# Kernel optimization log

Measured on AMD Instinct MI355X. Metric: run time of the kernel, lower is better.

Reference implementation:

```python
import jax, jax.numpy as jnp
import numpy as np

N_DIMS = 4
NEG_SLOPE = 0.01
ALPHA = 0.5

def leaky(v):
    return jnp.where(v > 0, v, NEG_SLOPE * v)

def gcn_conv(h, W, b, edge_index, n):
    """PyG GCNConv: add self-loops, symmetric normalization, then aggregate."""
    hw = h @ W  # [N, H]
    loops = jnp.arange(n, dtype=edge_index.dtype)
    src = jnp.concatenate([edge_index[0], loops])
    dst = jnp.concatenate([edge_index[1], loops])
    deg = jax.ops.segment_sum(jnp.ones_like(dst, dtype=hw.dtype), dst, num_segments=n)
    dinv = jnp.where(deg > 0, jax.lax.rsqrt(deg), 0.0)
    norm = dinv[src] * dinv[dst]  # [E+N]
    out = jax.ops.segment_sum(hw[src] * norm[:, None], dst, num_segments=n)
    return out + b

def setup_inputs() -> dict:
    key = jax.random.key(0)
    ks = jax.random.split(key, 8)
    N, IN, H, OUT, E = 50000, 512, 256, 512, 800000
    def kaiming(k, shape, fan_in):
        bound = np.sqrt(6.0 / fan_in)  # kaiming_uniform a=sqrt(5)-ish approx; gain sqrt(2)/sqrt(fan_in)*sqrt(3)
        bound = np.sqrt(2.0) * np.sqrt(3.0 / fan_in)
        return jax.random.uniform(k, shape, jnp.float32, -bound, bound)
    x = jax.random.normal(ks[0], (N, IN), jnp.float32)
    all_dim_edge_index = jax.random.randint(ks[1], (N_DIMS, 2, E), 0, N, jnp.int64)
    proj_mat = kaiming(ks[2], (N_DIMS, IN, H), IN)
    gcn_W = jax.random.uniform(ks[3], (N_DIMS, H, H), jnp.float32, -1, 1) * np.sqrt(1.0 / H)
    gcn_b = jnp.zeros((N_DIMS, H), jnp.float32)
    bilinear = kaiming(ks[4], (H, H), H)
    fan = H * N_DIMS
    inv_W = jax.random.uniform(ks[5], (fan, OUT), jnp.float32, -np.sqrt(1.0 / fan), np.sqrt(1.0 / fan))
    inv_b = jax.random.uniform(ks[6], (OUT,), jnp.float32, -np.sqrt(1.0 / fan), np.sqrt(1.0 / fan))
    return {"x": x, "all_dim_edge_index": all_dim_edge_index, "proj_mat": proj_mat,
            "gcn_W": gcn_W, "gcn_b": gcn_b, "bilinear": bilinear, "inv_W": inv_W, "inv_b": inv_b}

def reference(x, all_dim_edge_index, proj_mat, gcn_W, gcn_b, bilinear, inv_W, inv_b):
    n = x.shape[0]
    # per-dimension projection: [n_dims, N, H]
    dim_repr = leaky(jnp.einsum('ni,dih->dnh', x, proj_mat))
    # within-dimension GCN message passing (loop over small fixed n_dims)
    within_aggr = jnp.stack([
        gcn_conv(dim_repr[d], gcn_W[d], gcn_b[d], all_dim_edge_index[d], n)
        for d in range(N_DIMS)])
    # cross-dimension attention
    attention = jnp.einsum('aji,ik,bjk->ab', proj_mat, bilinear, proj_mat)
    attention = jax.nn.softmax(attention, axis=0)
    across_aggr = jnp.einsum('ab,anh->bnh', attention, dim_repr)
    new_dim_repr = ALPHA * within_aggr + (1.0 - ALPHA) * across_aggr  # [n_dims, N, H]
    concat = jnp.transpose(new_dim_repr, (1, 0, 2)).reshape(n, -1)  # [N, n_dims*H]
    return leaky(concat @ inv_W + inv_b)
```

## Files before the change

### kernel.cpp

```cpp
#include <hip/hip_runtime.h>
#include <math.h>

constexpr int N_NODES = 50000;
constexpr int IN_F    = 512;
constexpr int H_F     = 256;
constexpr int OUT_F   = 512;
constexpr int N_EDGE  = 800000;
constexpr int NDIM    = 4;
constexpr long NH     = (long)N_NODES * H_F;

#define LEAKY_SLOPE 0.01f

__device__ __forceinline__ float leaky_f(float v) { return v > 0.0f ? v : LEAKY_SLOPE * v; }

typedef __bf16 bf16x8 __attribute__((ext_vector_type(8)));
typedef float  f32x4  __attribute__((ext_vector_type(4)));

__device__ __forceinline__ void gload16(const void* g, void* s) {
  __builtin_amdgcn_global_load_lds(
      (const __attribute__((address_space(1))) void*)g,
      (__attribute__((address_space(3))) void*)s, 16, 0, 0);
}

template<bool AF32>
__global__ __launch_bounds__(256) void gemm_k(
    const float* __restrict__ Af, int ldaf,
    const __bf16* __restrict__ A1h, const __bf16* __restrict__ A1l, int lda1,
    const __bf16* __restrict__ A2h, const __bf16* __restrict__ A2l, int lda2, int kSplit,
    const __bf16* __restrict__ BhT, const __bf16* __restrict__ BlT,
    float* __restrict__ C, int ldc,
    const float* __restrict__ biasVec,
    __bf16* __restrict__ Oh, __bf16* __restrict__ Ol, int ldo,
    int M, int N, int K, int accumulate, int leaky)
{
  __shared__ __bf16 Ash[128][32];
  __shared__ __bf16 Asl[128][32];
  __shared__ __bf16 Bsh[128][32];
  __shared__ __bf16 Bsl[128][32];

  const int tid  = threadIdx.x;
  const int lane = tid & 63;
  const int wid  = tid >> 6;
  const int wm   = wid & 1;
  const int wn   = wid >> 1;
  const int l15  = lane & 15;
  const int quad = lane >> 4;
  const int col0 = blockIdx.x * 128;
  const int row0 = blockIdx.y * 128;

  f32x4 acc[4][4] = {};
  const int nkt = K >> 5;

  for (int kt = 0; kt < nkt; ++kt) {
    const int kk = kt << 5;
    __syncthreads();

    if constexpr (AF32) {
      #pragma unroll
      for (int p = 0; p < 4; ++p) {
        const int m = (tid >> 3) + p * 32;
        int row = row0 + m; row = row < M ? row : M - 1;
        const float4 v = *(const float4*)(Af + (size_t)row * ldaf + kk + (tid & 7) * 4);
        const float f[4] = {v.x, v.y, v.z, v.w};
        union { __bf16 b[4]; short4 s; } hh, ll;
        #pragma unroll
        for (int i = 0; i < 4; ++i) {
          const __bf16 hb = (__bf16)f[i];
          hh.b[i] = hb;
          ll.b[i] = (__bf16)(f[i] - (float)hb);
        }
        *(short4*)&Ash[m][(tid & 7) * 4] = hh.s;
        *(short4*)&Asl[m][(tid & 7) * 4] = ll.s;
      }
    } else {
      const __bf16* Ah; const __bf16* Al; int lda, k0;
      if (kk < kSplit) { Ah = A1h; Al = A1l; lda = lda1; k0 = kk; }
      else             { Ah = A2h; Al = A2l; lda = lda2; k0 = kk - kSplit; }
      #pragma unroll
      for (int p = 0; p < 2; ++p) {
        const int c = tid + p * 256;
        int row = row0 + (c >> 2); row = row < M ? row : M - 1;
        const size_t go = (size_t)row * lda + k0 + (c & 3) * 8;
        gload16(Ah + go, (__bf16*)Ash + (size_t)c * 8);
        gload16(Al + go, (__bf16*)Asl + (size_t)c * 8);
      }
    }
    #pragma unroll
    for (int p = 0; p < 2; ++p) {
      const int c = tid + p * 256;
      const int nn = col0 + (c >> 2);
      const size_t go = (size_t)nn * K + kk + (c & 3) * 8;
      gload16(BhT + go, (__bf16*)Bsh + (size_t)c * 8);
      gload16(BlT + go, (__bf16*)Bsl + (size_t)c * 8);
    }
    __syncthreads();

    bf16x8 ah[4], al[4], bh[4], bl[4];
    #pragma unroll
    for (int t = 0; t < 4; ++t) {
      ah[t] = *(const bf16x8*)&Ash[wm * 64 + t * 16 + l15][quad * 8];
      al[t] = *(const bf16x8*)&Asl[wm * 64 + t * 16 + l15][quad * 8];
      bh[t] = *(const bf16x8*)&Bsh[wn * 64 + t * 16 + l15][quad * 8];
      bl[t] = *(const bf16x8*)&Bsl[wn * 64 + t * 16 + l15][quad * 8];
    }
    #pragma unroll
    for (int mt = 0; mt < 4; ++mt)
      #pragma unroll
      for (int nt = 0; nt < 4; ++nt) {
        acc[mt][nt] = __builtin_amdgcn_mfma_f32_16x16x32_bf16(ah[mt], bh[nt], acc[mt][nt], 0, 0, 0);
        acc[mt][nt] = __builtin_amdgcn_mfma_f32_16x16x32_bf16(ah[mt], bl[nt], acc[mt][nt], 0, 0, 0);
        acc[mt][nt] = __builtin_amdgcn_mfma_f32_16x16x32_bf16(al[mt], bh[nt], acc[mt][nt], 0, 0, 0);
      }
  }

  #pragma unroll
  for (int mt = 0; mt < 4; ++mt)
    #pragma unroll
    for (int nt = 0; nt < 4; ++nt) {
      const int col = col0 + wn * 64 + nt * 16 + l15;
      const float bv = biasVec ? biasVec[col] : 0.0f;
      #pragma unroll
      for (int r = 0; r < 4; ++r) {
        const int row = row0 + wm * 64 + mt * 16 + quad * 4 + r;
        if (row < M) {
          float v = acc[mt][nt][r] + bv;
          if (accumulate) v += C[(size_t)row * ldc + col];
          if (leaky) v = leaky_f(v);
          if (Oh) {
            const __bf16 hv = (__bf16)v;
            Oh[(size_t)row * ldo + col] = hv;
            Ol[(size_t)row * ldo + col] = (__bf16)(v - (float)hv);
          } else {
            C[(size_t)row * ldc + col] = v;
          }
        }
      }
    }
}

__global__ void splitT_kernel(const float* __restrict__ B, __bf16* __restrict__ h,
                              __bf16* __restrict__ l, int Kd, int Nd, int total)
{
  int i = blockIdx.x * 256 + threadIdx.x;
  if (i >= total) return;
  int z   = i / (Kd * Nd);
  int rem = i - z * (Kd * Nd);
  int k = rem / Nd;
  int n = rem - k * Nd;
  float v = B[i];
  __bf16 hv = (__bf16)v;
  long o = (long)z * Kd * Nd + (long)n * Kd + k;
  h[o] = hv;
  l[o] = (__bf16)(v - (float)hv);
}

__global__ void splitA_kernel(const float* __restrict__ A, __bf16* __restrict__ h,
                              __bf16* __restrict__ l, long total)
{
  long i = (long)blockIdx.x * 256 + threadIdx.x;
  if (i >= total) return;
  float v = A[i];
  __bf16 hv = (__bf16)v;
  h[i] = hv;
  l[i] = (__bf16)(v - (float)hv);
}

__global__ void bcat_kernel(const float* __restrict__ invW, const float* __restrict__ att,
                            __bf16* __restrict__ h, __bf16* __restrict__ l)
{
  int i = blockIdx.x * 256 + threadIdx.x;
  if (i >= NDIM * OUT_F * 512) return;
  int d   = i >> 18;
  int rem = i & 262143;
  int n = rem >> 9;
  int k = rem & 511;
  float v;
  if (k < H_F) {
    v = invW[(long)(d * H_F + k) * OUT_F + n];
  } else {
    float s = 0.f;
    #pragma unroll
    for (int b = 0; b < 4; ++b)
      s += att[d * 4 + b] * invW[(long)(b * H_F + (k - H_F)) * OUT_F + n];
    v = 0.5f * s;
  }
  __bf16 hv = (__bf16)v;
  h[i] = hv;
  l[i] = (__bf16)(v - (float)hv);
}

__global__ void deg_count_kernel(const int* __restrict__ edges, int* __restrict__ cnt, int E)
{
  int i = blockIdx.x * 256 + threadIdx.x;
  if (i >= NDIM * E) return;
  int d = i / E;
  int e = i - d * E;
  int t = edges[(long)d * 2 * E + E + e];
  atomicAdd(&cnt[d * N_NODES + t], 1);
}

__global__ __launch_bounds__(1024) void scan_kernel(const int* __restrict__ cnt,
                                                    int* __restrict__ row_start,
                                                    float* __restrict__ dinv)
{
  const int d    = blockIdx.x;
  const int tid  = threadIdx.x;
  const int lane = tid & 63;
  const int wid  = tid >> 6;
  __shared__ int wsum[16];
  __shared__ int carry_s;
  if (tid == 0) carry_s = 0;
  __syncthreads();
  for (int base = 0; base < N_NODES; base += 1024) {
    int i = base + tid;
    int v = (i < N_NODES) ? cnt[d * N_NODES + i] : 0;
    if (i < N_NODES) dinv[d * N_NODES + i] = sqrtf(0.5f / (float)(v + 1));
    int incl = v;
    #pragma unroll
    for (int off = 1; off < 64; off <<= 1) {
      int nb = __shfl_up(incl, off, 64);
      if (lane >= off) incl += nb;
    }
    if (lane == 63) wsum[wid] = incl;
    __syncthreads();
    if (wid == 0 && lane < 16) {
      int s = wsum[lane];
      #pragma unroll
      for (int off = 1; off < 16; off <<= 1) {
        int nb = __shfl_up(s, off, 16);
        if (lane >= off) s += nb;
      }
      wsum[lane] = s;
    }
    __syncthreads();
    int waveoff = (wid == 0) ? 0 : wsum[wid - 1];
    if (i < N_NODES) row_start[d * (N_NODES + 1) + i] = carry_s + waveoff + incl - v;
    __syncthreads();
    if (tid == 1023) carry_s += wsum[15];
    __syncthreads();
  }
  if (tid == 0) row_start[d * (N_NODES + 1) + N_NODES] = carry_s;
}

__global__ void fill_kernel(const int* __restrict__ edges, const int* __restrict__ row_start,
                            int* __restrict__ fill_cnt, int* __restrict__ csr_src, int E)
{
  int i = blockIdx.x * 256 + threadIdx.x;
  if (i >= NDIM * E) return;
  int d = i / E;
  int e = i - d * E;
  int s = edges[(long)d * 2 * E + e];
  int t = edges[(long)d * 2 * E + E + e];
  int pos = row_start[d * (N_NODES + 1) + t] + atomicAdd(&fill_cnt[d * N_NODES + t], 1);
  csr_src[(long)d * E + pos] = s;
}

__global__ __launch_bounds__(256) void gather_aggr_kernel(
    const float* __restrict__ hw, const int* __restrict__ csr_src,
    const int* __restrict__ row_start, const float* __restrict__ dinv,
    const float* __restrict__ bias, __bf16* __restrict__ Wh, __bf16* __restrict__ Wl)
{
  const int n = blockIdx.x * 4 + (threadIdx.x >> 6);
  const int lane = threadIdx.x & 63;
  const float dt = dinv[n];
  const float sl = dt * dt;
  const float4 b = *(const float4*)(bias + lane * 4);
  const float4 h = *(const float4*)(hw + (size_t)n * H_F + lane * 4);
  float4 a0 = make_float4(0.5f * b.x + sl * h.x, 0.5f * b.y + sl * h.y,
                          0.5f * b.z + sl * h.z, 0.5f * b.w + sl * h.w);
  float4 a1 = make_float4(0.f, 0.f, 0.f, 0.f);
  const int beg = row_start[n];
  const int end = row_start[n + 1];
  int j = beg;
  for (; j + 2 <= end; j += 2) {
    const int s0 = csr_src[j];
    const int s1 = csr_src[j + 1];
    const float nm0 = dt * dinv[s0];
    const float nm1 = dt * dinv[s1];
    const float4 v0 = *(const float4*)(hw + (size_t)s0 * H_F + lane * 4);
    const float4 v1 = *(const float4*)(hw + (size_t)s1 * H_F + lane * 4);
    a0.x = fmaf(nm0, v0.x, a0.x); a0.y = fmaf(nm0, v0.y, a0.y);
    a0.z = fmaf(nm0, v0.z, a0.z); a0.w = fmaf(nm0, v0.w, a0.w);
    a1.x = fmaf(nm1, v1.x, a1.x); a1.y = fmaf(nm1, v1.y, a1.y);
    a1.z = fmaf(nm1, v1.z, a1.z); a1.w = fmaf(nm1, v1.w, a1.w);
  }
  if (j < end) {
    const int s0 = csr_src[j];
    const float nm0 = dt * dinv[s0];
    const float4 v0 = *(const float4*)(hw + (size_t)s0 * H_F + lane * 4);
    a0.x = fmaf(nm0, v0.x, a0.x); a0.y = fmaf(nm0, v0.y, a0.y);
    a0.z = fmaf(nm0, v0.z, a0.z); a0.w = fmaf(nm0, v0.w, a0.w);
  }
  const float av[4] = {a0.x + a1.x, a0.y + a1.y, a0.z + a1.z, a0.w + a1.w};
  union { __bf16 b[4]; short4 s; } H, L;
  #pragma unroll
  for (int i = 0; i < 4; ++i) {
    const __bf16 hv = (__bf16)av[i];
    H.b[i] = hv;
    L.b[i] = (__bf16)(av[i] - (float)hv);
  }
  *(short4*)(Wh + (size_t)n * H_F + lane * 4) = H.s;
  *(short4*)(Wl + (size_t)n * H_F + lane * 4) = L.s;
}

__global__ void att_dot_kernel(const float* __restrict__ T, const float* __restrict__ P,
                               float* __restrict__ out16)
{
  const int a = blockIdx.x >> 2;
  const int b = blockIdx.x & 3;
  const float* ta = T + (long)a * (IN_F * H_F);
  const float* pb = P + (long)b * (IN_F * H_F);
  float s = 0.f;
  for (int i = threadIdx.x; i < IN_F * H_F; i += 256) s += ta[i] * pb[i];
  #pragma unroll
  for (int off = 32; off > 0; off >>= 1) s += __shfl_down(s, off, 64);
  __shared__ float red[4];
  if ((threadIdx.x & 63) == 0) red[threadIdx.x >> 6] = s;
  __syncthreads();
  if (threadIdx.x == 0) out16[blockIdx.x] = red[0] + red[1] + red[2] + red[3];
}

__global__ void att_softmax_kernel(const float* __restrict__ raw, float* __restrict__ att)
{
  int b = threadIdx.x;
  if (b < 4) {
    float r0 = raw[b], r1 = raw[4 + b], r2 = raw[8 + b], r3 = raw[12 + b];
    float m = fmaxf(fmaxf(r0, r1), fmaxf(r2, r3));
    float e0 = expf(r0 - m), e1 = expf(r1 - m), e2 = expf(r2 - m), e3 = expf(r3 - m);
    float inv = 1.0f / (e0 + e1 + e2 + e3);
    att[b] = e0 * inv; att[4 + b] = e1 * inv; att[8 + b] = e2 * inv; att[12 + b] = e3 * inv;
  }
}

extern "C" void kernel_launch(void* const* d_in, const int* in_sizes, int n_in,
                              void* d_out, int out_size, void* d_ws, size_t ws_size,
                              hipStream_t stream)
{
  const float* x     = (const float*)d_in[0];
  const int*   edges = (const int*)d_in[1];
  const float* proj  = (const float*)d_in[2];
  const float* gcnW  = (const float*)d_in[3];
  const float* gcnB  = (const float*)d_in[4];
  const float* bil   = (const float*)d_in[5];
  const float* invW  = (const float*)d_in[6];
  const float* invB  = (const float*)d_in[7];
  float* out = (float*)d_out;

  float* HWB       = (float*)d_ws;
  float* dinv      = HWB + NH;
  float* Tbuf      = dinv + NDIM * N_NODES;
  float* att_raw   = Tbuf + (long)NDIM * IN_F * H_F;
  float* att       = att_raw + 16;
  int*   cnt       = (int*)(att + 16);
  int*   fill_cnt  = cnt + NDIM * N_NODES;
  int*   row_start = fill_cnt + NDIM * N_NODES;
  int*   csr_src   = row_start + NDIM * (N_NODES + 1);
  __bf16* projTh   = (__bf16*)(csr_src + (long)NDIM * N_EDGE);
  __bf16* projTl   = projTh + (long)NDIM * IN_F * H_F;
  __bf16* gcnWTh   = projTl + (long)NDIM * IN_F * H_F;
  __bf16* gcnWTl   = gcnWTh + (long)NDIM * H_F * H_F;
  __bf16* bcatTh   = gcnWTl + (long)NDIM * H_F * H_F;
  __bf16* bcatTl   = bcatTh + (long)NDIM * OUT_F * 512;
  __bf16* bilTh    = bcatTl + (long)NDIM * OUT_F * 512;
  __bf16* bilTl    = bilTh + (long)H_F * H_F;
  __bf16* Rh       = bilTl + (long)H_F * H_F;
  __bf16* Rl       = Rh + NH;
  __bf16* WBh      = Rl + NH;
  __bf16* WBl      = WBh + NH;
  __bf16* xh       = WBl + NH;
  __bf16* xl       = xh + (long)N_NODES * IN_F;
  const size_t need_x = (size_t)((char*)(xl + (long)N_NODES * IN_F) - (char*)d_ws);
  const bool XS = ws_size >= need_x;

  const int MBL = (N_NODES + 127) / 128;

  hipMemsetAsync(cnt, 0, (size_t)2 * NDIM * N_NODES * sizeof(int), stream);
  deg_count_kernel<<<(NDIM * N_EDGE + 255) / 256, 256, 0, stream>>>(edges, cnt, N_EDGE);
  scan_kernel<<<NDIM, 1024, 0, stream>>>(cnt, row_start, dinv);
  fill_kernel<<<(NDIM * N_EDGE + 255) / 256, 256, 0, stream>>>(edges, row_start, fill_cnt,
                                                               csr_src, N_EDGE);

  splitT_kernel<<<(NDIM * IN_F * H_F + 255) / 256, 256, 0, stream>>>(
      proj, projTh, projTl, IN_F, H_F, NDIM * IN_F * H_F);
  splitT_kernel<<<(NDIM * H_F * H_F + 255) / 256, 256, 0, stream>>>(
      gcnW, gcnWTh, gcnWTl, H_F, H_F, NDIM * H_F * H_F);
  splitT_kernel<<<(H_F * H_F + 255) / 256, 256, 0, stream>>>(
      bil, bilTh, bilTl, H_F, H_F, H_F * H_F);

  for (int a = 0; a < NDIM; ++a)
    gemm_k<true><<<dim3(H_F / 128, IN_F / 128), 256, 0, stream>>>(
        proj + (long)a * IN_F * H_F, H_F,
        nullptr, nullptr, 0, nullptr, nullptr, 0, 0,
        bilTh, bilTl,
        Tbuf + (long)a * IN_F * H_F, H_F,
        nullptr, nullptr, nullptr, 0,
        IN_F, H_F, H_F, 0, 0);
  att_dot_kernel<<<16, 256, 0, stream>>>(Tbuf, proj, att_raw);
  att_softmax_kernel<<<1, 64, 0, stream>>>(att_raw, att);
  bcat_kernel<<<(NDIM * OUT_F * 512 + 255) / 256, 256, 0, stream>>>(invW, att, bcatTh, bcatTl);

  if (XS)
    splitA_kernel<<<(int)(((long)N_NODES * IN_F + 255) / 256), 256, 0, stream>>>(
        x, xh, xl, (long)N_NODES * IN_F);

  for (int d = 0; d < NDIM; ++d) {
    if (XS)
      gemm_k<false><<<dim3(H_F / 128, MBL), 256, 0, stream>>>(
          nullptr, 0,
          xh, xl, IN_F, xh, xl, IN_F, IN_F,
          projTh + (long)d * IN_F * H_F, projTl + (long)d * IN_F * H_F,
          nullptr, 0, nullptr,
          Rh, Rl, H_F,
          N_NODES, H_F, IN_F, 0, 1);
    else
      gemm_k<true><<<dim3(H_F / 128, MBL), 256, 0, stream>>>(
          x, IN_F,
          nullptr, nullptr, 0, nullptr, nullptr, 0, 0,
          projTh + (long)d * IN_F * H_F, projTl + (long)d * IN_F * H_F,
          nullptr, 0, nullptr,
          Rh, Rl, H_F,
          N_NODES, H_F, IN_F, 0, 1);

    gemm_k<false><<<dim3(H_F / 128, MBL), 256, 0, stream>>>(
        nullptr, 0,
        Rh, Rl, H_F, Rh, Rl, H_F, H_F,
        gcnWTh + (long)d * H_F * H_F, gcnWTl + (long)d * H_F * H_F,
        HWB, H_F, nullptr,
        nullptr, nullptr, 0,
        N_NODES, H_F, H_F, 0, 0);

    gather_aggr_kernel<<<N_NODES / 4, 256, 0, stream>>>(
        HWB, csr_src + (long)d * N_EDGE, row_start + d * (N_NODES + 1),
        dinv + d * N_NODES, gcnB + d * H_F, WBh, WBl);

    gemm_k<false><<<dim3(OUT_F / 128, MBL), 256, 0, stream>>>(
        nullptr, 0,
        WBh, WBl, H_F, Rh, Rl, H_F, H_F,
        bcatTh + (long)d * OUT_F * 512, bcatTl + (long)d * OUT_F * 512,
        out, OUT_F, (d == 0) ? invB : nullptr,
        nullptr, nullptr, 0,
        N_NODES, OUT_F, 512, (d == 0) ? 0 : 1, (d == NDIM - 1) ? 1 : 0);
  }

  (void)in_sizes; (void)n_in; (void)out_size; (void)ws_size;
}
```

Baseline: 2.927 ms.

## Register-prefetch GEMM pipeline, XCD swizzle, and fused wide-K output GEMM

Replaces the direct global-to-LDS loads in the GEMM with register prefetch of the next K tile, overlapped with the MFMAs, and stores tiles in LDS with an XOR swizzle to avoid bank conflicts. Workgroups are remapped across the 8 XCDs. The output projection now runs as one GEMM over a wide concatenated [WB|R] buffer spanning up to all four dims, instead of four accumulating GEMMs. This cuts passes over the output. The x pre-split kernel is dropped in favour of converting fp32 to bf16 inside the GEMM, and the gather loop is unrolled to 4 edges. These add register pressure and two barriers per K step, and the wide buffer needs more workspace.

```diff
diff --git a/kernel.cpp b/kernel.cpp
--- a/kernel.cpp
+++ b/kernel.cpp
@@ -16,27 +16,29 @@
 typedef __bf16 bf16x8 __attribute__((ext_vector_type(8)));
 typedef float  f32x4  __attribute__((ext_vector_type(4)));
 
-__device__ __forceinline__ void gload16(const void* g, void* s) {
-  __builtin_amdgcn_global_load_lds(
-      (const __attribute__((address_space(1))) void*)g,
-      (__attribute__((address_space(3))) void*)s, 16, 0, 0);
+__device__ __forceinline__ void swz_block(int& mb, int& nb) {
+  const int nwg = (int)(gridDim.x * gridDim.y);
+  const int hw  = (int)(blockIdx.y * gridDim.x + blockIdx.x);
+  const int xcd = hw & 7, idx = hw >> 3;
+  const int q8 = nwg >> 3, r8 = nwg & 7;
+  const int wk = (xcd < r8 ? xcd * (q8 + 1) : r8 * (q8 + 1) + (xcd - r8) * q8) + idx;
+  nb = wk % (int)gridDim.x;
+  mb = wk / (int)gridDim.x;
 }
 
 template<bool AF32>
 __global__ __launch_bounds__(256) void gemm_k(
     const float* __restrict__ Af, int ldaf,
-    const __bf16* __restrict__ A1h, const __bf16* __restrict__ A1l, int lda1,
-    const __bf16* __restrict__ A2h, const __bf16* __restrict__ A2l, int lda2, int kSplit,
-    const __bf16* __restrict__ BhT, const __bf16* __restrict__ BlT,
-    float* __restrict__ C, int ldc,
-    const float* __restrict__ biasVec,
+    const __bf16* __restrict__ Ah, const __bf16* __restrict__ Al, int lda,
+    const __bf16* __restrict__ BhT, const __bf16* __restrict__ BlT, int ldb,
+    float* __restrict__ C, int ldc, const float* __restrict__ biasVec,
     __bf16* __restrict__ Oh, __bf16* __restrict__ Ol, int ldo,
-    int M, int N, int K, int accumulate, int leaky)
-{
-  __shared__ __bf16 Ash[128][32];
-  __shared__ __bf16 Asl[128][32];
-  __shared__ __bf16 Bsh[128][32];
-  __shared__ __bf16 Bsl[128][32];
+    int M, int K, int accumulate, int leaky)
+{
+  __shared__ __bf16 Ash[4096];
+  __shared__ __bf16 Asl[4096];
+  __shared__ __bf16 Bsh[4096];
+  __shared__ __bf16 Bsl[4096];
 
   const int tid  = threadIdx.x;
   const int lane = tid & 63;
@@ -45,72 +47,132 @@
   const int wn   = wid >> 1;
   const int l15  = lane & 15;
   const int quad = lane >> 4;
-  const int col0 = blockIdx.x * 128;
-  const int row0 = blockIdx.y * 128;
+
+  int mb, nb;
+  swz_block(mb, nb);
+  const int row0 = mb * 128;
+  const int col0 = nb * 128;
 
   f32x4 acc[4][4] = {};
   const int nkt = K >> 5;
 
+  int4   avh0, avh1, avl0, avl1;
+  int4   bvh0, bvh1, bvl0, bvl1;
+  float4 ar0, ar1, ar2, ar3;
+
+  const int rrB = tid >> 2;
+  const int qB  = tid & 3;
+
+  auto loadB = [&](int kt) {
+    const int kb = kt << 5;
+    const size_t s0 = (size_t)(col0 + rrB) * ldb + kb + qB * 8;
+    const size_t s1 = (size_t)(col0 + rrB + 64) * ldb + kb + qB * 8;
+    bvh0 = *(const int4*)(BhT + s0);
+    bvl0 = *(const int4*)(BlT + s0);
+    bvh1 = *(const int4*)(BhT + s1);
+    bvl1 = *(const int4*)(BlT + s1);
+  };
+  auto writeB = [&]() {
+    const int o0 = rrB * 32 + ((qB ^ ((rrB >> 1) & 3)) << 3);
+    const int r1 = rrB + 64;
+    const int o1 = r1 * 32 + ((qB ^ ((r1 >> 1) & 3)) << 3);
+    *(int4*)&Bsh[o0] = bvh0;
+    *(int4*)&Bsl[o0] = bvl0;
+    *(int4*)&Bsh[o1] = bvh1;
+    *(int4*)&Bsl[o1] = bvl1;
+  };
+  auto loadA16 = [&](int kt) {
+    const int kb = kt << 5;
+    int r0c = row0 + rrB;      r0c = r0c < M ? r0c : M - 1;
+    int r1c = row0 + rrB + 64; r1c = r1c < M ? r1c : M - 1;
+    const size_t s0 = (size_t)r0c * lda + kb + qB * 8;
+    const size_t s1 = (size_t)r1c * lda + kb + qB * 8;
+    avh0 = *(const int4*)(Ah + s0);
+    avl0 = *(const int4*)(Al + s0);
+    avh1 = *(const int4*)(Ah + s1);
+    avl1 = *(const int4*)(Al + s1);
+  };
+  auto writeA16 = [&]() {
+    const int o0 = rrB * 32 + ((qB ^ ((rrB >> 1) & 3)) << 3);
+    const int r1 = rrB + 64;
+    const int o1 = r1 * 32 + ((qB ^ ((r1 >> 1) & 3)) << 3);
+    *(int4*)&Ash[o0] = avh0;
+    *(int4*)&Asl[o0] = avl0;
+    *(int4*)&Ash[o1] = avh1;
+    *(int4*)&Asl[o1] = avl1;
+  };
+  auto loadA32 = [&](int kt) {
+    const int kb = (kt << 5) + (tid & 7) * 4;
+    const int m  = tid >> 3;
+    int r;
+    r = row0 + m;      r = r < M ? r : M - 1; ar0 = *(const float4*)(Af + (size_t)r * ldaf + kb);
+    r = row0 + m + 32; r = r < M ? r : M - 1; ar1 = *(const float4*)(Af + (size_t)r * ldaf + kb);
+    r = row0 + m + 64; r = r < M ? r : M - 1; ar2 = *(const float4*)(Af + (size_t)r * ldaf + kb);
+    r = row0 + m + 96; r = r < M ? r : M - 1; ar3 = *(const float4*)(Af + (size_t)r * ldaf + kb);
+  };
+  auto writeA32 = [&]() {
+    const int q16 = (tid & 7) >> 1;
+    const int sub = (tid & 1) * 4;
+    const int m0  = tid >> 3;
+    const float4 regs[4] = {ar0, ar1, ar2, ar3};
+    #pragma unroll
+    for (int p = 0; p < 4; ++p) {
+      const int m = m0 + p * 32;
+      const float f[4] = {regs[p].x, regs[p].y, regs[p].z, regs[p].w};
+      union { __bf16 b[4]; short4 s; } hh, ll;
+      #pragma unroll
+      for (int i = 0; i < 4; ++i) {
+        const __bf16 hb = (__bf16)f[i];
+        hh.b[i] = hb;
+        ll.b[i] = (__bf16)(f[i] - (float)hb);
+      }
+      const int off = m * 32 + ((q16 ^ ((m >> 1) & 3)) << 3) + sub;
+      *(short4*)&Ash[off] = hh.s;
+      *(short4*)&Asl[off] = ll.s;
+    }
+  };
+
+  if constexpr (AF32) { loadA32(0); } else { loadA16(0); }
+  loadB(0);
+  if constexpr (AF32) { writeA32(); } else { writeA16(); }
+  writeB();
+  __syncthreads();
+
   for (int kt = 0; kt < nkt; ++kt) {
-    const int kk = kt << 5;
-    __syncthreads();
-
-    if constexpr (AF32) {
-      #pragma unroll
-      for (int p = 0; p < 4; ++p) {
-        const int m = (tid >> 3) + p * 32;
-        int row = row0 + m; row = row < M ? row : M - 1;
-        const float4 v = *(const float4*)(Af + (size_t)row * ldaf + kk + (tid & 7) * 4);
-        const float f[4] = {v.x, v.y, v.z, v.w};
-        union { __bf16 b[4]; short4 s; } hh, ll;
-        #pragma unroll
-        for (int i = 0; i < 4; ++i) {
-          const __bf16 hb = (__bf16)f[i];
-          hh.b[i] = hb;
-          ll.b[i] = (__bf16)(f[i] - (float)hb);
-        }
-        *(short4*)&Ash[m][(tid & 7) * 4] = hh.s;
-        *(short4*)&Asl[m][(tid & 7) * 4] = ll.s;
-      }
-    } else {
-      const __bf16* Ah; const __bf16* Al; int lda, k0;
-      if (kk < kSplit) { Ah = A1h; Al = A1l; lda = lda1; k0 = kk; }
-      else             { Ah = A2h; Al = A2l; lda = lda2; k0 = kk - kSplit; }
-      #pragma unroll
-      for (int p = 0; p < 2; ++p) {
-        const int c = tid + p * 256;
-        int row = row0 + (c >> 2); row = row < M ? row : M - 1;
-        const size_t go = (size_t)row * lda + k0 + (c & 3) * 8;
-        gload16(Ah + go, (__bf16*)Ash + (size_t)c * 8);
-        gload16(Al + go, (__bf16*)Asl + (size_t)c * 8);
-      }
-    }
-    #pragma unroll
-    for (int p = 0; p < 2; ++p) {
-      const int c = tid + p * 256;
-      const int nn = col0 + (c >> 2);
-      const size_t go = (size_t)nn * K + kk + (c & 3) * 8;
-      gload16(BhT + go, (__bf16*)Bsh + (size_t)c * 8);
-      gload16(BlT + go, (__bf16*)Bsl + (size_t)c * 8);
-    }
-    __syncthreads();
-
-    bf16x8 ah[4], al[4], bh[4], bl[4];
+    bf16x8 fah[4], fal[4], fbh[4], fbl[4];
     #pragma unroll
     for (int t = 0; t < 4; ++t) {
-      ah[t] = *(const bf16x8*)&Ash[wm * 64 + t * 16 + l15][quad * 8];
-      al[t] = *(const bf16x8*)&Asl[wm * 64 + t * 16 + l15][quad * 8];
-      bh[t] = *(const bf16x8*)&Bsh[wn * 64 + t * 16 + l15][quad * 8];
-      bl[t] = *(const bf16x8*)&Bsl[wn * 64 + t * 16 + l15][quad * 8];
-    }
+      const int ar = wm * 64 + t * 16 + l15;
+      const int br = wn * 64 + t * 16 + l15;
+      const int as = ar * 32 + ((quad ^ ((ar >> 1) & 3)) << 3);
+      const int bs = br * 32 + ((quad ^ ((br >> 1) & 3)) << 3);
+      fah[t] = *(const bf16x8*)&Ash[as];
+      fal[t] = *(const bf16x8*)&Asl[as];
+      fbh[t] = *(const bf16x8*)&Bsh[bs];
+      fbl[t] = *(const bf16x8*)&Bsl[bs];
+    }
+
+    const bool more = (kt + 1) < nkt;
+    if (more) {
+      if constexpr (AF32) { loadA32(kt + 1); } else { loadA16(kt + 1); }
+      loadB(kt + 1);
+    }
+
     #pragma unroll
     for (int mt = 0; mt < 4; ++mt)
       #pragma unroll
       for (int nt = 0; nt < 4; ++nt) {
-        acc[mt][nt] = __builtin_amdgcn_mfma_f32_16x16x32_bf16(ah[mt], bh[nt], acc[mt][nt], 0, 0, 0);
-        acc[mt][nt] = __builtin_amdgcn_mfma_f32_16x16x32_bf16(ah[mt], bl[nt], acc[mt][nt], 0, 0, 0);
-        acc[mt][nt] = __builtin_amdgcn_mfma_f32_16x16x32_bf16(al[mt], bh[nt], acc[mt][nt], 0, 0, 0);
+        acc[mt][nt] = __builtin_amdgcn_mfma_f32_16x16x32_bf16(fah[mt], fbh[nt], acc[mt][nt], 0, 0, 0);
+        acc[mt][nt] = __builtin_amdgcn_mfma_f32_16x16x32_bf16(fah[mt], fbl[nt], acc[mt][nt], 0, 0, 0);
+        acc[mt][nt] = __builtin_amdgcn_mfma_f32_16x16x32_bf16(fal[mt], fbh[nt], acc[mt][nt], 0, 0, 0);
       }
+
+    __syncthreads();
+    if (more) {
+      if constexpr (AF32) { writeA32(); } else { writeA16(); }
+      writeB();
+    }
+    __syncthreads();
   }
 
   #pragma unroll
@@ -154,17 +216,6 @@
   l[o] = (__bf16)(v - (float)hv);
 }
 
-__global__ void splitA_kernel(const float* __restrict__ A, __bf16* __restrict__ h,
-                              __bf16* __restrict__ l, long total)
-{
-  long i = (long)blockIdx.x * 256 + threadIdx.x;
-  if (i >= total) return;
-  float v = A[i];
-  __bf16 hv = (__bf16)v;
-  h[i] = hv;
-  l[i] = (__bf16)(v - (float)hv);
-}
-
 __global__ void bcat_kernel(const float* __restrict__ invW, const float* __restrict__ att,
                             __bf16* __restrict__ h, __bf16* __restrict__ l)
 {
@@ -185,8 +236,9 @@
     v = 0.5f * s;
   }
   __bf16 hv = (__bf16)v;
-  h[i] = hv;
-  l[i] = (__bf16)(v - (float)hv);
+  long o = (long)n * (NDIM * 512) + d * 512 + k;
+  h[o] = hv;
+  l[o] = (__bf16)(v - (float)hv);
 }
 
 __global__ void deg_count_kernel(const int* __restrict__ edges, int* __restrict__ cnt, int E)
@@ -258,7 +310,8 @@
 __global__ __launch_bounds__(256) void gather_aggr_kernel(
     const float* __restrict__ hw, const int* __restrict__ csr_src,
     const int* __restrict__ row_start, const float* __restrict__ dinv,
-    const float* __restrict__ bias, __bf16* __restrict__ Wh, __bf16* __restrict__ Wl)
+    const float* __restrict__ bias, __bf16* __restrict__ Wh, __bf16* __restrict__ Wl,
+    int ldw)
 {
   const int n = blockIdx.x * 4 + (threadIdx.x >> 6);
   const int lane = threadIdx.x & 63;
@@ -269,29 +322,42 @@
   float4 a0 = make_float4(0.5f * b.x + sl * h.x, 0.5f * b.y + sl * h.y,
                           0.5f * b.z + sl * h.z, 0.5f * b.w + sl * h.w);
   float4 a1 = make_float4(0.f, 0.f, 0.f, 0.f);
+  float4 a2 = make_float4(0.f, 0.f, 0.f, 0.f);
+  float4 a3 = make_float4(0.f, 0.f, 0.f, 0.f);
   const int beg = row_start[n];
   const int end = row_start[n + 1];
   int j = beg;
-  for (; j + 2 <= end; j += 2) {
+  for (; j + 4 <= end; j += 4) {
     const int s0 = csr_src[j];
     const int s1 = csr_src[j + 1];
+    const int s2 = csr_src[j + 2];
+    const int s3 = csr_src[j + 3];
     const float nm0 = dt * dinv[s0];
     const float nm1 = dt * dinv[s1];
+    const float nm2 = dt * dinv[s2];
+    const float nm3 = dt * dinv[s3];
     const float4 v0 = *(const float4*)(hw + (size_t)s0 * H_F + lane * 4);
     const float4 v1 = *(const float4*)(hw + (size_t)s1 * H_F + lane * 4);
+    const float4 v2 = *(const float4*)(hw + (size_t)s2 * H_F + lane * 4);
+    const float4 v3 = *(const float4*)(hw + (size_t)s3 * H_F + lane * 4);
     a0.x = fmaf(nm0, v0.x, a0.x); a0.y = fmaf(nm0, v0.y, a0.y);
     a0.z = fmaf(nm0, v0.z, a0.z); a0.w = fmaf(nm0, v0.w, a0.w);
     a1.x = fmaf(nm1, v1.x, a1.x); a1.y = fmaf(nm1, v1.y, a1.y);
     a1.z = fmaf(nm1, v1.z, a1.z); a1.w = fmaf(nm1, v1.w, a1.w);
-  }
-  if (j < end) {
+    a2.x = fmaf(nm2, v2.x, a2.x); a2.y = fmaf(nm2, v2.y, a2.y);
+    a2.z = fmaf(nm2, v2.z, a2.z); a2.w = fmaf(nm2, v2.w, a2.w);
+    a3.x = fmaf(nm3, v3.x, a3.x); a3.y = fmaf(nm3, v3.y, a3.y);
+    a3.z = fmaf(nm3, v3.z, a3.z); a3.w = fmaf(nm3, v3.w, a3.w);
+  }
+  for (; j < end; ++j) {
     const int s0 = csr_src[j];
     const float nm0 = dt * dinv[s0];
     const float4 v0 = *(const float4*)(hw + (size_t)s0 * H_F + lane * 4);
     a0.x = fmaf(nm0, v0.x, a0.x); a0.y = fmaf(nm0, v0.y, a0.y);
     a0.z = fmaf(nm0, v0.z, a0.z); a0.w = fmaf(nm0, v0.w, a0.w);
   }
-  const float av[4] = {a0.x + a1.x, a0.y + a1.y, a0.z + a1.z, a0.w + a1.w};
+  const float av[4] = {a0.x + a1.x + a2.x + a3.x, a0.y + a1.y + a2.y + a3.y,
+                       a0.z + a1.z + a2.z + a3.z, a0.w + a1.w + a2.w + a3.w};
   union { __bf16 b[4]; short4 s; } H, L;
   #pragma unroll
   for (int i = 0; i < 4; ++i) {
@@ -299,8 +365,8 @@
     H.b[i] = hv;
     L.b[i] = (__bf16)(av[i] - (float)hv);
   }
-  *(short4*)(Wh + (size_t)n * H_F + lane * 4) = H.s;
-  *(short4*)(Wl + (size_t)n * H_F + lane * 4) = L.s;
+  *(short4*)(Wh + (size_t)n * ldw + lane * 4) = H.s;
+  *(short4*)(Wl + (size_t)n * ldw + lane * 4) = L.s;
 }
 
 __global__ void att_dot_kernel(const float* __restrict__ T, const float* __restrict__ P,
@@ -363,14 +429,17 @@
   __bf16* bcatTl   = bcatTh + (long)NDIM * OUT_F * 512;
   __bf16* bilTh    = bcatTl + (long)NDIM * OUT_F * 512;
   __bf16* bilTl    = bilTh + (long)H_F * H_F;
-  __bf16* Rh       = bilTl + (long)H_F * H_F;
-  __bf16* Rl       = Rh + NH;
-  __bf16* WBh      = Rl + NH;
-  __bf16* WBl      = WBh + NH;
-  __bf16* xh       = WBl + NH;
-  __bf16* xl       = xh + (long)N_NODES * IN_F;
-  const size_t need_x = (size_t)((char*)(xl + (long)N_NODES * IN_F) - (char*)d_ws);
-  const bool XS = ws_size >= need_x;
+  __bf16* fatH     = bilTl + (long)H_F * H_F;
+
+  const size_t base_bytes = (size_t)((char*)fatH - (char*)d_ws);
+  auto fatBytes = [](int ktot) { return (size_t)2 * N_NODES * ktot * sizeof(__bf16); };
+  int KTOT;
+  if      (ws_size >= base_bytes + fatBytes(2048)) KTOT = 2048;
+  else if (ws_size >= base_bytes + fatBytes(1024)) KTOT = 1024;
+  else                                             KTOT = 512;
+  const int DPG  = KTOT / 512;
+  const int NGEN = NDIM / DPG;
+  __bf16* fatL = fatH + (size_t)N_NODES * KTOT;
 
   const int MBL = (N_NODES + 127) / 128;
 
@@ -390,57 +459,52 @@
   for (int a = 0; a < NDIM; ++a)
     gemm_k<true><<<dim3(H_F / 128, IN_F / 128), 256, 0, stream>>>(
         proj + (long)a * IN_F * H_F, H_F,
-        nullptr, nullptr, 0, nullptr, nullptr, 0, 0,
-        bilTh, bilTl,
-        Tbuf + (long)a * IN_F * H_F, H_F,
-        nullptr, nullptr, nullptr, 0,
-        IN_F, H_F, H_F, 0, 0);
+        nullptr, nullptr, 0,
+        bilTh, bilTl, H_F,
+        Tbuf + (long)a * IN_F * H_F, H_F, nullptr,
+        nullptr, nullptr, 0,
+        IN_F, H_F, 0, 0);
   att_dot_kernel<<<16, 256, 0, stream>>>(Tbuf, proj, att_raw);
   att_softmax_kernel<<<1, 64, 0, stream>>>(att_raw, att);
   bcat_kernel<<<(NDIM * OUT_F * 512 + 255) / 256, 256, 0, stream>>>(invW, att, bcatTh, bcatTl);
 
-  if (XS)
-    splitA_kernel<<<(int)(((long)N_NODES * IN_F + 255) / 256), 256, 0, stream>>>(
-        x, xh, xl, (long)N_NODES * IN_F);
-
-  for (int d = 0; d < NDIM; ++d) {
-    if (XS)
+  for (int g = 0; g < NGEN; ++g) {
+    for (int j = 0; j < DPG; ++j) {
+      const int d = g * DPG + j;
+      __bf16* wbH = fatH + j * 512;
+      __bf16* wbL = fatL + j * 512;
+      __bf16* rH  = fatH + j * 512 + 256;
+      __bf16* rL  = fatL + j * 512 + 256;
+
+      gemm_k<true><<<dim3(H_F / 128, MBL), 256, 0, stream>>>(
+          x, IN_F,
+          nullptr, nullptr, 0,
+          projTh + (long)d * IN_F * H_F, projTl + (long)d * IN_F * H_F, IN_F,
+          nullptr, 0, nullptr,
+          rH, rL, KTOT,
+          N_NODES, IN_F, 0, 1);
+
       gemm_k<false><<<dim3(H_F / 128, MBL), 256, 0, stream>>>(
           nullptr, 0,
-          xh, xl, IN_F, xh, xl, IN_F, IN_F,
-          projTh + (long)d * IN_F * H_F, projTl + (long)d * IN_F * H_F,
-          nullptr, 0, nullptr,
-          Rh, Rl, H_F,
-          N_NODES, H_F, IN_F, 0, 1);
-    else
-      gemm_k<true><<<dim3(H_F / 128, MBL), 256, 0, stream>>>(
-          x, IN_F,
-          nullptr, nullptr, 0, nullptr, nullptr, 0, 0,
-          projTh + (long)d * IN_F * H_F, projTl + (long)d * IN_F * H_F,
-          nullptr, 0, nullptr,
-          Rh, Rl, H_F,
-          N_NODES, H_F, IN_F, 0, 1);
-
-    gemm_k<false><<<dim3(H_F / 128, MBL), 256, 0, stream>>>(
-        nullptr, 0,
-        Rh, Rl, H_F, Rh, Rl, H_F, H_F,
-        gcnWTh + (long)d * H_F * H_F, gcnWTl + (long)d * H_F * H_F,
-        HWB, H_F, nullptr,
-        nullptr, nullptr, 0,
-        N_NODES, H_F, H_F, 0, 0);
-
-    gather_aggr_kernel<<<N_NODES / 4, 256, 0, stream>>>(
-        HWB, csr_src + (long)d * N_EDGE, row_start + d * (N_NODES + 1),
-        dinv + d * N_NODES, gcnB + d * H_F, WBh, WBl);
+          rH, rL, KTOT,
+          gcnWTh + (long)d * H_F * H_F, gcnWTl + (long)d * H_F * H_F, H_F,
+          HWB, H_F, nullptr,
+          nullptr, nullptr, 0,
+          N_NODES, H_F, 0, 0);
+
+      gather_aggr_kernel<<<N_NODES / 4, 256, 0, stream>>>(
+          HWB, csr_src + (long)d * N_EDGE, row_start + d * (N_NODES + 1),
+          dinv + d * N_NODES, gcnB + d * H_F, wbH, wbL, KTOT);
+    }
 
     gemm_k<false><<<dim3(OUT_F / 128, MBL), 256, 0, stream>>>(
         nullptr, 0,
-        WBh, WBl, H_F, Rh, Rl, H_F, H_F,
-        bcatTh + (long)d * OUT_F * 512, bcatTl + (long)d * OUT_F * 512,
-        out, OUT_F, (d == 0) ? invB : nullptr,
+        fatH, fatL, KTOT,
+        bcatTh + (long)g * KTOT, bcatTl + (long)g * KTOT, NDIM * 512,
+        out, OUT_F, (g == 0) ? invB : nullptr,
         nullptr, nullptr, 0,
-        N_NODES, OUT_F, 512, (d == 0) ? 0 : 1, (d == NDIM - 1) ? 1 : 0);
-  }
-
-  (void)in_sizes; (void)n_in; (void)out_size; (void)ws_size;
-}
+        N_NODES, KTOT, (g == 0) ? 0 : 1, (g == NGEN - 1) ? 1 : 0);
+  }
+
+  (void)in_sizes; (void)n_in; (void)out_size;
+}
```

Result: faster. 2.446 ms (-16.4%).
